# Optimization experiments

Hardware: AMD Instinct MI355X
Metric: run time of the kernel (lower is better)

The kernel has to match this reference:

```python
import jax, jax.numpy as jnp
import numpy as np

D = 768        # d_model
NH = 12        # n_head
HD = D // NH   # head_dim = 64
T = 8          # num_frames
SCALE = 1.0
LN_EPS = 1e-5


def _layer_norm(x, g, b):
    # fp16-safe LayerNorm: compute in fp32, cast back (matches LayerNorm subclass)
    x32 = x.astype(jnp.float32)
    mu = jnp.mean(x32, axis=-1, keepdims=True)
    var = jnp.mean(jnp.square(x32 - mu), axis=-1, keepdims=True)
    y = (x32 - mu) / jnp.sqrt(var + LN_EPS) * g + b
    return y.astype(x.dtype)


def _adapter(x, w1, b1, w2, b2):
    # Adapter with skip_connect=False: fc1 -> exact GELU -> fc2
    h = jax.nn.gelu(x @ w1.T + b1, approximate=False)
    return h @ w2.T + b2


def _mha(xq, ykv, w_in, b_in, w_out, b_out, need_weights=False):
    # xq: (Tx, N, D), ykv: (Ty, N, D); manual in-proj split like the torch code
    q = xq @ w_in[:D].T + b_in[:D]
    k = ykv @ w_in[D:2 * D].T + b_in[D:2 * D]
    v = ykv @ w_in[2 * D:].T + b_in[2 * D:]
    Tx, N = q.shape[0], q.shape[1]
    Ty = k.shape[0]
    q = q.reshape(Tx, N, NH, HD).transpose(1, 2, 0, 3)  # (N, H, Tx, hd)
    k = k.reshape(Ty, N, NH, HD).transpose(1, 2, 0, 3)
    v = v.reshape(Ty, N, NH, HD).transpose(1, 2, 0, 3)
    aff = jnp.einsum('nhqd,nhkd->nhqk', q, k) / jnp.asarray(HD ** 0.5, q.dtype)
    if need_weights:
        # torch does this under no_grad: sum over heads, exp, sum over (Tx*Ty)
        w = jax.lax.stop_gradient(
            jnp.sum(jnp.exp(jnp.sum(aff, axis=1)).reshape(N, -1), axis=-1))
    p = jax.nn.softmax(aff, axis=-1)
    out = jnp.einsum('nhqk,nhkd->nhqd', p, v)
    out = out.transpose(2, 0, 1, 3).reshape(Tx, N, D)
    out = out @ w_out.T + b_out
    if need_weights:
        return out, w
    return out


def setup_inputs() -> dict:
    key = jax.random.key(0)
    ks = jax.random.split(key, 12)
    DH = D // 4  # adapter hidden = 192

    def w(k, shape):
        return jax.random.normal(k, shape, jnp.float32) * 0.02

    z = lambda *s: jnp.zeros(s, jnp.float32)
    return {
        'x': jax.random.normal(ks[0], (197, 64, D), jnp.float32),
        'in_proj_w': w(ks[1], (3 * D, D)), 'in_proj_b': z(3 * D),
        'out_proj_w': w(ks[2], (D, D)), 'out_proj_b': z(D),
        'ln1_g': jnp.ones((D,), jnp.float32), 'ln1_b': z(D),
        'ln2_g': jnp.ones((D,), jnp.float32), 'ln2_b': z(D),
        'fc_w': w(ks[3], (4 * D, D)), 'fc_b': z(4 * D),
        'proj_w': w(ks[4], (D, 4 * D)), 'proj_b': z(D),
        'sa1_w': w(ks[5], (DH, D)), 'sa1_b': z(DH),
        'sa2_w': w(ks[6], (D, DH)), 'sa2_b': z(D),
        'ta1_w': w(ks[7], (DH, D)), 'ta1_b': z(DH),
        'ta2_w': w(ks[8], (D, DH)), 'ta2_b': z(D),
        'ma1_w': w(ks[9], (DH, D)), 'ma1_b': z(DH),
        'ma2_w': w(ks[10], (D, DH)), 'ma2_b': z(D),
    }


def reference(x, in_proj_w, in_proj_b, out_proj_w, out_proj_b,
              ln1_g, ln1_b, ln2_g, ln2_b, fc_w, fc_b, proj_w, proj_b,
              sa1_w, sa1_b, sa2_w, sa2_b, ta1_w, ta1_b, ta2_w, ta2_b,
              ma1_w, ma1_b, ma2_w, ma2_b):
    n, bt, d = x.shape
    b = bt // T
    # temporal attention on the class token: 'n (b t) d -> t (b n) d'
    ct = x[0]                                   # (bt, d)
    xt = ct.reshape(b, T, d).transpose(1, 0, 2)  # (T, b, d)
    xt = _mha(_layer_norm(xt, ln1_g, ln1_b), _layer_norm(xt, ln1_g, ln1_b),
              in_proj_w, in_proj_b, out_proj_w, out_proj_b)
    xt = _adapter(xt, ta1_w, ta1_b, ta2_w, ta2_b)
    xt = xt.transpose(1, 0, 2).reshape(1, bt, d)  # 't (b n) d -> n (b t) d'

    xln = _layer_norm(x, ln1_g, ln1_b)
    ori_attn, ori_w = _mha(xln, xln, in_proj_w, in_proj_b,
                           out_proj_w, out_proj_b, need_weights=True)
    crs_attn, crs_w = _mha(xln, xt, in_proj_w, in_proj_b,
                           out_proj_w, out_proj_b, need_weights=True)
    lam = (crs_w / (crs_w + ori_w))[None, :, None]  # (1, bt, 1)
    x = x + (1.0 - lam) * ori_attn \
          + SCALE * _adapter(lam * crs_attn, sa1_w, sa1_b, sa2_w, sa2_b)

    xn = _layer_norm(x, ln2_g, ln2_b)
    h = xn @ fc_w.T + fc_b
    h = h * jax.nn.sigmoid(1.702 * h)  # QuickGELU
    mlp_out = h @ proj_w.T + proj_b
    x = x + mlp_out + SCALE * _adapter(xn, ma1_w, ma1_b, ma2_w, ma2_b)
    return x
```

## Files before the change

kernel.cpp:

```cpp
#include <hip/hip_runtime.h>
#include <hip/hip_bf16.h>
#include <math.h>


typedef __attribute__((ext_vector_type(8))) short bf16x8;
typedef __attribute__((ext_vector_type(4))) float f32x4;

__device__ __forceinline__ float bf2f(short s) {
  unsigned u = ((unsigned)(unsigned short)s) << 16;
  float f;
  __builtin_memcpy(&f, &u, 4);
  return f;
}
__device__ __forceinline__ short f2bf(float f) {
  __hip_bfloat16 h = __float2bfloat16(f);
  short s;
  __builtin_memcpy(&s, &h, 2);
  return s;
}

__device__ __forceinline__ void gld16(void* lds, const void* g) {
  __builtin_amdgcn_global_load_lds(
      (const __attribute__((address_space(1))) unsigned int*)g,
      (__attribute__((address_space(3))) unsigned int*)lds, 16, 0, 0);
}

struct WPair { const float* s; short* d; int n; };
struct WArr { WPair p[10]; };

__global__ __launch_bounds__(256)
void convert_k(WArr a) {
  WPair w = a.p[blockIdx.y];
  for (int i = blockIdx.x * 256 + threadIdx.x; i < w.n; i += gridDim.x * 256)
    w.d[i] = f2bf(w.s[i]);
}

__global__ __launch_bounds__(256)
void ln_k(const float* __restrict__ in, const float* __restrict__ g,
          const float* __restrict__ b, short* __restrict__ out) {
  const int t = blockIdx.x;
  const float* xr = in + (size_t)t * 768;
  const int tid = threadIdx.x;
  float v0 = xr[tid], v1 = xr[tid + 256], v2 = xr[tid + 512];
  float s = v0 + v1 + v2;
#pragma unroll
  for (int m = 1; m < 64; m <<= 1) s += __shfl_xor(s, m);
  __shared__ float red[4];
  if ((tid & 63) == 0) red[tid >> 6] = s;
  __syncthreads();
  float mu = (red[0] + red[1] + red[2] + red[3]) * (1.f / 768.f);
  __syncthreads();
  float d0 = v0 - mu, d1 = v1 - mu, d2 = v2 - mu;
  float q = d0 * d0 + d1 * d1 + d2 * d2;
#pragma unroll
  for (int m = 1; m < 64; m <<= 1) q += __shfl_xor(q, m);
  if ((tid & 63) == 0) red[tid >> 6] = q;
  __syncthreads();
  float rstd = rsqrtf((red[0] + red[1] + red[2] + red[3]) * (1.f / 768.f) + 1e-5f);
  size_t o = (size_t)t * 768;
  out[o + tid]       = f2bf(d0 * rstd * g[tid]       + b[tid]);
  out[o + tid + 256] = f2bf(d1 * rstd * g[tid + 256] + b[tid + 256]);
  out[o + tid + 512] = f2bf(d2 * rstd * g[tid + 512] + b[tid + 512]);
}

template <int ACT, int EPI>
__global__ __launch_bounds__(256)
void gemm_k(const short* __restrict__ A, int lda,
            const short* __restrict__ W,
            const float* __restrict__ bias,
            short* __restrict__ outb, float* __restrict__ outf,
            const float* __restrict__ lam,
            int M, int N, int K) {
  __shared__ short As[64][40];
  __shared__ short Ws[64][40];
  const int tid = threadIdx.x;
  const int n0 = blockIdx.x * 64;
  const int m0 = blockIdx.y * 64;
  const int lane = tid & 63, w = tid >> 6;
  const int wr = w >> 1, wc = w & 1;
  const int g = lane >> 4, li = lane & 15;
  const int srow = tid >> 2, scol = (tid & 3) * 8;

  f32x4 acc[2][2];
#pragma unroll
  for (int i = 0; i < 2; i++)
#pragma unroll
    for (int j = 0; j < 2; j++) acc[i][j] = (f32x4){0.f, 0.f, 0.f, 0.f};

  const short* Aptr = A + (size_t)(m0 + srow) * lda + scol;
  const short* Wptr = W + (size_t)(n0 + srow) * K + scol;

  for (int kk = 0; kk < K; kk += 32) {
    __syncthreads();
    *(bf16x8*)&As[srow][scol] = *(const bf16x8*)(Aptr + kk);
    *(bf16x8*)&Ws[srow][scol] = *(const bf16x8*)(Wptr + kk);
    __syncthreads();
    bf16x8 a[2], b[2];
#pragma unroll
    for (int mi = 0; mi < 2; ++mi)
      a[mi] = *(const bf16x8*)&As[wr * 32 + mi * 16 + li][g * 8];
#pragma unroll
    for (int ni = 0; ni < 2; ++ni)
      b[ni] = *(const bf16x8*)&Ws[wc * 32 + ni * 16 + li][g * 8];
#pragma unroll
    for (int mi = 0; mi < 2; ++mi)
#pragma unroll
      for (int ni = 0; ni < 2; ++ni)
        acc[mi][ni] = __builtin_amdgcn_mfma_f32_16x16x32_bf16(
            a[mi], b[ni], acc[mi][ni], 0, 0, 0);
  }

#pragma unroll
  for (int mi = 0; mi < 2; ++mi)
#pragma unroll
    for (int ni = 0; ni < 2; ++ni)
#pragma unroll
      for (int r = 0; r < 4; ++r) {
        int row = m0 + wr * 32 + mi * 16 + g * 4 + r;
        int col = n0 + wc * 32 + ni * 16 + li;
        float v = acc[mi][ni][r];
        if (bias) v += bias[col];
        if (ACT == 1) v = v / (1.f + __expf(-1.702f * v));
        if (ACT == 2) v = 0.5f * v * (1.f + erff(v * 0.70710678118f));
        size_t idx = (size_t)row * N + col;
        if (EPI == 0) outb[idx] = f2bf(v);
        else if (EPI == 1) outf[idx] = v;
        else if (EPI == 5) outb[idx] = f2bf(v * lam[row]);
      }
}

template <int ACT, int EPI>
__global__ __launch_bounds__(256)
void gemm128p_k(const short* __restrict__ A, int lda,
                const short* __restrict__ W,
                const float* __restrict__ bias,
                short* __restrict__ outb, float* __restrict__ outf,
                const float* __restrict__ lam,
                const float* __restrict__ addv,
                const float* __restrict__ resid,
                const short* __restrict__ A2, int lda2,
                const short* __restrict__ W2,
                const float* __restrict__ bias2, int K2,
                int M, int N, int K, int nx) {
  int nwg = gridDim.x;
  int orig = blockIdx.x;
  int q = nwg >> 3, r = nwg & 7;
  int xcd = orig & 7, cidx = orig >> 3;
  int wgid = (xcd < r ? xcd * (q + 1) : r * (q + 1) + (xcd - r) * q) + cidx;
  const int n0 = (wgid % nx) * 128;
  const int m0 = (wgid / nx) * 128;

  __shared__ short As[3][128][32];
  __shared__ short Ws[3][128][32];
  const int tid = threadIdx.x;
  const int w = tid >> 6, lane = tid & 63;
  const int g = lane >> 4, li = lane & 15;
  const int wr = w >> 1, wc = w & 1;

  const int srow = w * 16 + (lane >> 2);
  const int scol = (lane & 3) * 8;

  f32x4 acc[4][4];
#pragma unroll
  for (int i = 0; i < 4; i++)
#pragma unroll
    for (int j = 0; j < 4; j++) acc[i][j] = (f32x4){0.f, 0.f, 0.f, 0.f};

  int ar0 = m0 + srow;       if (ar0 > M - 1) ar0 = M - 1;
  int ar1 = m0 + 64 + srow;  if (ar1 > M - 1) ar1 = M - 1;
  const short* Ap0 = A + (size_t)ar0 * lda + scol;
  const short* Ap1 = A + (size_t)ar1 * lda + scol;
  const short* Wp0 = W + (size_t)(n0 + srow) * K + scol;
  const short* Wp1 = W + (size_t)(n0 + 64 + srow) * K + scol;
  const short* A2b = A2 ? A2 : A;
  const short* W2b = W2 ? W2 : W;
  const short* Bp0 = A2b + (size_t)ar0 * lda2 + scol;
  const short* Bp1 = A2b + (size_t)ar1 * lda2 + scol;
  const short* Vp0 = W2b + (size_t)(n0 + srow) * K2 + scol;
  const short* Vp1 = W2b + (size_t)(n0 + 64 + srow) * K2 + scol;

  const int ks1 = K >> 5;
  const int ks2 = A2 ? (K2 >> 5) : 0;
  const int total = ks1 + ks2;

  auto STAGE = [&](int s, int bi) {
    if (s < ks1) {
      const int kk = s * 32;
      gld16(&As[bi][w * 16][0],      Ap0 + kk);
      gld16(&As[bi][64 + w * 16][0], Ap1 + kk);
      gld16(&Ws[bi][w * 16][0],      Wp0 + kk);
      gld16(&Ws[bi][64 + w * 16][0], Wp1 + kk);
    } else {
      const int kk = (s - ks1) * 32;
      gld16(&As[bi][w * 16][0],      Bp0 + kk);
      gld16(&As[bi][64 + w * 16][0], Bp1 + kk);
      gld16(&Ws[bi][w * 16][0],      Vp0 + kk);
      gld16(&Ws[bi][64 + w * 16][0], Vp1 + kk);
    }
  };

  STAGE(0, 0);
  STAGE(1, 1);

  int bi = 0;
  for (int t = 0; t < total; ++t) {
    if (t + 1 < total)
      asm volatile("s_waitcnt vmcnt(4)" ::: "memory");
    else
      asm volatile("s_waitcnt vmcnt(0)" ::: "memory");
    __builtin_amdgcn_s_barrier();

    int nb = bi + 2; if (nb >= 3) nb -= 3;
    if (t + 2 < total) STAGE(t + 2, nb);

    bf16x8 a[4], b[4];
#pragma unroll
    for (int mi = 0; mi < 4; ++mi)
      a[mi] = *(const bf16x8*)&As[bi][wr * 64 + mi * 16 + li][g * 8];
#pragma unroll
    for (int ni = 0; ni < 4; ++ni)
      b[ni] = *(const bf16x8*)&Ws[bi][wc * 64 + ni * 16 + li][g * 8];
    asm volatile("s_waitcnt lgkmcnt(0)" ::: "memory");
    __builtin_amdgcn_sched_barrier(0);
#pragma unroll
    for (int mi = 0; mi < 4; ++mi)
#pragma unroll
      for (int ni = 0; ni < 4; ++ni)
        acc[mi][ni] = __builtin_amdgcn_mfma_f32_16x16x32_bf16(
            a[mi], b[ni], acc[mi][ni], 0, 0, 0);

    bi = bi + 1; if (bi >= 3) bi = 0;
  }

#pragma unroll
  for (int mi = 0; mi < 4; ++mi)
#pragma unroll
    for (int ni = 0; ni < 4; ++ni)
#pragma unroll
      for (int r = 0; r < 4; ++r) {
        int row = m0 + wr * 64 + mi * 16 + g * 4 + r;
        int col = n0 + wc * 64 + ni * 16 + li;
        if (row >= M) continue;
        float v = acc[mi][ni][r];
        if (bias) v += bias[col];
        if (bias2) v += bias2[col];
        if (ACT == 1) v = v / (1.f + __expf(-1.702f * v));
        if (ACT == 2) v = 0.5f * v * (1.f + erff(v * 0.70710678118f));
        size_t idx = (size_t)row * N + col;
        if (EPI == 0) outb[idx] = f2bf(v);
        else if (EPI == 2) {
          float l = lam[row & 63];
          outf[idx] = resid[idx] + (1.f - l) * v + addv[(size_t)(row & 63) * 768 + col];
        } else if (EPI == 6) outf[idx] = resid[idx] + v;
      }
}

__global__ __launch_bounds__(256)
void attn_k(const short* __restrict__ qkv, short* __restrict__ attn_out) {
  const int n = blockIdx.x;
  const int h = blockIdx.y;
  const int tid = threadIdx.x;
  const int lane = tid & 63, w = tid >> 6;
  const int g = lane >> 4, li = lane & 15;

  __shared__ short Vt[64][232];
  __shared__ short Pl[4][16][232];

  {
    const int d = tid & 63;
    for (int key = tid >> 6; key < 224; key += 4) {
      short v = 0;
      if (key < 197)
        v = qkv[(size_t)(key * 64 + n) * 2304 + 1536 + h * 64 + d];
      Vt[d][key] = v;
    }
  }
  __syncthreads();

  const short* Qb = qkv + (size_t)n * 2304 + h * 64;
  const short* Kb = Qb + 768;

  for (int mt = w; mt < 13; mt += 4) {
    const int m0 = mt * 16;
    int arow = m0 + li;
    if (arow > 196) arow = 196;
    bf16x8 a0 = *(const bf16x8*)(Qb + (size_t)arow * 147456 + g * 8);
    bf16x8 a1 = *(const bf16x8*)(Qb + (size_t)arow * 147456 + 32 + g * 8);

    float s[13][4];
#pragma unroll
    for (int nt = 0; nt < 13; ++nt) {
      int kc = nt * 16 + li;
      if (kc > 196) kc = 196;
      bf16x8 b0 = *(const bf16x8*)(Kb + (size_t)kc * 147456 + g * 8);
      bf16x8 b1 = *(const bf16x8*)(Kb + (size_t)kc * 147456 + 32 + g * 8);
      f32x4 acc = (f32x4){0.f, 0.f, 0.f, 0.f};
      acc = __builtin_amdgcn_mfma_f32_16x16x32_bf16(a0, b0, acc, 0, 0, 0);
      acc = __builtin_amdgcn_mfma_f32_16x16x32_bf16(a1, b1, acc, 0, 0, 0);
#pragma unroll
      for (int r = 0; r < 4; ++r) s[nt][r] = acc[r] * 0.125f;
    }

#pragma unroll
    for (int r = 0; r < 4; ++r) {
      float mx = -1e30f;
#pragma unroll
      for (int nt = 0; nt < 13; ++nt) {
        if (nt * 16 + li >= 197) s[nt][r] = -1e30f;
        mx = fmaxf(mx, s[nt][r]);
      }
      mx = fmaxf(mx, __shfl_xor(mx, 1));
      mx = fmaxf(mx, __shfl_xor(mx, 2));
      mx = fmaxf(mx, __shfl_xor(mx, 4));
      mx = fmaxf(mx, __shfl_xor(mx, 8));
      float sum = 0.f;
#pragma unroll
      for (int nt = 0; nt < 13; ++nt) {
        float e = (s[nt][r] <= -1e29f) ? 0.f : __expf(s[nt][r] - mx);
        s[nt][r] = e;
        sum += e;
      }
      sum += __shfl_xor(sum, 1);
      sum += __shfl_xor(sum, 2);
      sum += __shfl_xor(sum, 4);
      sum += __shfl_xor(sum, 8);
      float inv = 1.f / sum;
#pragma unroll
      for (int nt = 0; nt < 13; ++nt) s[nt][r] *= inv;
    }

#pragma unroll
    for (int r = 0; r < 4; ++r) {
      int row = g * 4 + r;
#pragma unroll
      for (int nt = 0; nt < 13; ++nt)
        Pl[w][row][nt * 16 + li] = f2bf(s[nt][r]);
      Pl[w][row][208 + li] = 0;
    }
    asm volatile("s_waitcnt lgkmcnt(0)" ::: "memory");
    __builtin_amdgcn_sched_barrier(0);

    f32x4 o[4];
#pragma unroll
    for (int ni = 0; ni < 4; ++ni) o[ni] = (f32x4){0.f, 0.f, 0.f, 0.f};
#pragma unroll
    for (int kk = 0; kk < 7; ++kk) {
      bf16x8 pa = *(const bf16x8*)&Pl[w][li][kk * 32 + g * 8];
#pragma unroll
      for (int ni = 0; ni < 4; ++ni) {
        bf16x8 vb = *(const bf16x8*)&Vt[ni * 16 + li][kk * 32 + g * 8];
        o[ni] = __builtin_amdgcn_mfma_f32_16x16x32_bf16(pa, vb, o[ni], 0, 0, 0);
      }
    }
#pragma unroll
    for (int ni = 0; ni < 4; ++ni)
#pragma unroll
      for (int r = 0; r < 4; ++r) {
        int prow = m0 + g * 4 + r;
        if (prow < 197)
          attn_out[(size_t)(prow * 64 + n) * 768 + h * 64 + ni * 16 + li] =
              f2bf(o[ni][r]);
      }
  }
}

__global__ __launch_bounds__(256)
void lam_part_k(const short* __restrict__ qkv, float* __restrict__ eo_part) {
  const int n = blockIdx.x;
  const int mt = blockIdx.y;
  const int tid = threadIdx.x;
  const int lane = tid & 63, w = tid >> 6;
  const int g = lane >> 4, li = lane & 15;
  const short* Qb = qkv + (size_t)n * 2304;
  const short* Kb = Qb + 768;

  int arow = mt * 16 + li;
  if (arow > 196) arow = 196;
  const short* Ap = Qb + (size_t)arow * 147456;

  bf16x8 a[24];
#pragma unroll
  for (int s = 0; s < 24; ++s)
    a[s] = *(const bf16x8*)(Ap + s * 32 + g * 8);

  float eo = 0.f;
  for (int nt = w; nt < 13; nt += 4) {
    int kc = nt * 16 + li;
    if (kc > 196) kc = 196;
    const short* Bp = Kb + (size_t)kc * 147456;
    f32x4 acc = (f32x4){0.f, 0.f, 0.f, 0.f};
#pragma unroll
    for (int s = 0; s < 24; ++s) {
      bf16x8 b = *(const bf16x8*)(Bp + s * 32 + g * 8);
      acc = __builtin_amdgcn_mfma_f32_16x16x32_bf16(a[s], b, acc, 0, 0, 0);
    }
#pragma unroll
    for (int r = 0; r < 4; ++r) {
      int prow = mt * 16 + g * 4 + r;
      int col = nt * 16 + li;
      if (prow < 197 && col < 197) eo += __expf(acc[r] * 0.125f);
    }
  }

#pragma unroll
  for (int m = 1; m < 64; m <<= 1) eo += __shfl_xor(eo, m);
  __shared__ float red[4];
  if (lane == 0) red[w] = eo;
  __syncthreads();
  if (tid == 0)
    eo_part[n * 13 + mt] = red[0] + red[1] + red[2] + red[3];
}

__global__ __launch_bounds__(64)
void lam_fin_k(const short* __restrict__ qkv, const short* __restrict__ kvt,
               const float* __restrict__ eo_part, float* __restrict__ lam) {
  const int n = blockIdx.x;
  const int lane = threadIdx.x;
  const short* kt = kvt + (size_t)n * 1536;

  float ec = 0.f;
  for (int p = lane; p < 197; p += 64) {
    const short* qp = qkv + (size_t)n * 2304 + (size_t)p * 147456;
    float dot = 0.f;
    for (int d0 = 0; d0 < 768; d0 += 8) {
      bf16x8 qa = *(const bf16x8*)(qp + d0);
      bf16x8 ka = *(const bf16x8*)(kt + d0);
#pragma unroll
      for (int j = 0; j < 8; ++j) dot += bf2f(qa[j]) * bf2f(ka[j]);
    }
    ec += __expf(dot * 0.125f);
  }
#pragma unroll
  for (int m = 1; m < 64; m <<= 1) ec += __shfl_xor(ec, m);

  if (lane == 0) {
    float eo = 0.f;
#pragma unroll
    for (int t = 0; t < 13; ++t) eo += eo_part[n * 13 + t];
    lam[n] = ec / (ec + eo);
  }
}

__global__ __launch_bounds__(64)
void tattn_k(const short* __restrict__ qkv, short* __restrict__ attn_t) {
  const int bb = blockIdx.x, h = blockIdx.y;
  const int tid = threadIdx.x;
  __shared__ float sm[8][9];
  {
    const int tt = tid >> 3, ss = tid & 7;
    const short* q = qkv + (size_t)(bb * 8 + tt) * 2304 + h * 64;
    const short* k = qkv + (size_t)(bb * 8 + ss) * 2304 + 768 + h * 64;
    float dot = 0.f;
#pragma unroll
    for (int d = 0; d < 64; d += 8) {
      bf16x8 qa = *(const bf16x8*)(q + d);
      bf16x8 ka = *(const bf16x8*)(k + d);
#pragma unroll
      for (int j = 0; j < 8; ++j) dot += bf2f(qa[j]) * bf2f(ka[j]);
    }
    sm[tt][ss] = dot * 0.125f;
  }
  __syncthreads();
  if (tid < 8) {
    float mx = -1e30f;
#pragma unroll
    for (int s2 = 0; s2 < 8; ++s2) mx = fmaxf(mx, sm[tid][s2]);
    float sum = 0.f;
#pragma unroll
    for (int s2 = 0; s2 < 8; ++s2) {
      float e = __expf(sm[tid][s2] - mx);
      sm[tid][s2] = e;
      sum += e;
    }
    float inv = 1.f / sum;
#pragma unroll
    for (int s2 = 0; s2 < 8; ++s2) sm[tid][s2] *= inv;
  }
  __syncthreads();
  {
    const int d = tid;
    float v[8];
#pragma unroll
    for (int s2 = 0; s2 < 8; ++s2)
      v[s2] = bf2f(qkv[(size_t)(bb * 8 + s2) * 2304 + 1536 + h * 64 + d]);
#pragma unroll
    for (int tt = 0; tt < 8; ++tt) {
      float o = 0.f;
#pragma unroll
      for (int s2 = 0; s2 < 8; ++s2) o += sm[tt][s2] * v[s2];
      attn_t[(size_t)(bb * 8 + tt) * 768 + h * 64 + d] = f2bf(o);
    }
  }
}

extern "C" void kernel_launch(void* const* d_in, const int* in_sizes, int n_in,
                              void* d_out, int out_size, void* d_ws,
                              size_t ws_size, hipStream_t stream) {
  (void)in_sizes; (void)n_in; (void)out_size; (void)ws_size;

  const float* x          = (const float*)d_in[0];
  const float* in_proj_w  = (const float*)d_in[1];
  const float* in_proj_b  = (const float*)d_in[2];
  const float* out_proj_w = (const float*)d_in[3];
  const float* out_proj_b = (const float*)d_in[4];
  const float* ln1_g      = (const float*)d_in[5];
  const float* ln1_b      = (const float*)d_in[6];
  const float* ln2_g      = (const float*)d_in[7];
  const float* ln2_b      = (const float*)d_in[8];
  const float* fc_w       = (const float*)d_in[9];
  const float* fc_b       = (const float*)d_in[10];
  const float* proj_w     = (const float*)d_in[11];
  const float* proj_b     = (const float*)d_in[12];
  const float* sa1_w      = (const float*)d_in[13];
  const float* sa1_b      = (const float*)d_in[14];
  const float* sa2_w      = (const float*)d_in[15];
  const float* sa2_b      = (const float*)d_in[16];
  const float* ta1_w      = (const float*)d_in[17];
  const float* ta1_b      = (const float*)d_in[18];
  const float* ta2_w      = (const float*)d_in[19];
  const float* ta2_b      = (const float*)d_in[20];
  const float* ma1_w      = (const float*)d_in[21];
  const float* ma1_b      = (const float*)d_in[22];
  const float* ma2_w      = (const float*)d_in[23];
  const float* ma2_b      = (const float*)d_in[24];

  char* ws = (char*)d_ws;
  short* xln  = (short*)(ws + 0);
  short* qkv  = (short*)(ws + 19365888);
  short* hbuf = (short*)(ws + 0);
  short* attn = (short*)(ws + 77463552);
  short* h2   = (short*)(ws + 77463552);
  float* x1   = (float*)(ws + 96829440);
  short* xn   = (short*)(ws + 135561216);

  char* wreg = ws + 154927104;
  short* w_inproj  = (short*)(wreg + 0);
  short* w_outproj = (short*)(wreg + 3538944);
  short* w_fc      = (short*)(wreg + 4718592);
  short* w_proj    = (short*)(wreg + 9437184);
  short* w_sa1     = (short*)(wreg + 14155776);
  short* w_sa2     = (short*)(wreg + 14450688);
  short* w_ta1     = (short*)(wreg + 14745600);
  short* w_ta2     = (short*)(wreg + 15040512);
  short* w_ma1     = (short*)(wreg + 15335424);
  short* w_ma2     = (short*)(wreg + 15630336);

  char* sm = ws + 170852352;
  short* attn_t  = (short*)(sm + 0);
  short* tproj   = (short*)(sm + 98304);
  short* th      = (short*)(sm + 196608);
  short* xt_out  = (short*)(sm + 221184);
  short* kv_t    = (short*)(sm + 319488);
  short* a_in    = (short*)(sm + 516096);
  short* sa_h    = (short*)(sm + 614400);
  float* sa_out  = (float*)(sm + 638976);
  float* lam     = (float*)(sm + 835584);
  float* eo_part = (float*)(sm + 835840);

  float* out = (float*)d_out;

  WArr arr;
  arr.p[0] = {in_proj_w,  w_inproj,  2304 * 768};
  arr.p[1] = {out_proj_w, w_outproj, 768 * 768};
  arr.p[2] = {fc_w,       w_fc,      3072 * 768};
  arr.p[3] = {proj_w,     w_proj,    768 * 3072};
  arr.p[4] = {sa1_w,      w_sa1,     192 * 768};
  arr.p[5] = {sa2_w,      w_sa2,     768 * 192};
  arr.p[6] = {ta1_w,      w_ta1,     192 * 768};
  arr.p[7] = {ta2_w,      w_ta2,     768 * 192};
  arr.p[8] = {ma1_w,      w_ma1,     192 * 768};
  arr.p[9] = {ma2_w,      w_ma2,     768 * 192};
  convert_k<<<dim3(128, 10), 256, 0, stream>>>(arr);

  ln_k<<<12608, 256, 0, stream>>>(x, ln1_g, ln1_b, xln);

  gemm128p_k<0, 0><<<18 * 99, 256, 0, stream>>>(
      xln, 768, w_inproj, in_proj_b, qkv, nullptr, nullptr, nullptr, nullptr,
      nullptr, 0, nullptr, nullptr, 32, 12608, 2304, 768, 18);

  lam_part_k<<<dim3(64, 13), 256, 0, stream>>>(qkv, eo_part);

  tattn_k<<<dim3(8, 12), 64, 0, stream>>>(qkv, attn_t);

  gemm_k<0, 0><<<dim3(12, 1), 256, 0, stream>>>(
      attn_t, 768, w_outproj, out_proj_b, tproj, nullptr, nullptr, 64, 768, 768);
  gemm_k<2, 0><<<dim3(3, 1), 256, 0, stream>>>(
      tproj, 768, w_ta1, ta1_b, th, nullptr, nullptr, 64, 192, 768);
  gemm_k<0, 0><<<dim3(12, 1), 256, 0, stream>>>(
      th, 192, w_ta2, ta2_b, xt_out, nullptr, nullptr, 64, 768, 192);
  gemm_k<0, 0><<<dim3(24, 1), 256, 0, stream>>>(
      xt_out, 768, w_inproj + 768 * 768, in_proj_b + 768, kv_t, nullptr,
      nullptr, 64, 1536, 768);

  attn_k<<<dim3(64, 12), 256, 0, stream>>>(qkv, attn);

  lam_fin_k<<<64, 64, 0, stream>>>(qkv, kv_t, eo_part, lam);

  gemm_k<0, 5><<<dim3(12, 1), 256, 0, stream>>>(
      kv_t + 768, 1536, w_outproj, out_proj_b, a_in, nullptr, lam, 64, 768, 768);
  gemm_k<2, 0><<<dim3(3, 1), 256, 0, stream>>>(
      a_in, 768, w_sa1, sa1_b, sa_h, nullptr, nullptr, 64, 192, 768);
  gemm_k<0, 1><<<dim3(12, 1), 256, 0, stream>>>(
      sa_h, 192, w_sa2, sa2_b, nullptr, sa_out, nullptr, 64, 768, 192);

  gemm128p_k<0, 2><<<6 * 99, 256, 0, stream>>>(
      attn, 768, w_outproj, out_proj_b, nullptr, x1, lam, sa_out, x,
      nullptr, 0, nullptr, nullptr, 32, 12608, 768, 768, 6);

  ln_k<<<12608, 256, 0, stream>>>(x1, ln2_g, ln2_b, xn);

  gemm128p_k<1, 0><<<24 * 99, 256, 0, stream>>>(
      xn, 768, w_fc, fc_b, hbuf, nullptr, nullptr, nullptr, nullptr,
      nullptr, 0, nullptr, nullptr, 32, 12608, 3072, 768, 24);
  gemm_k<2, 0><<<dim3(3, 197), 256, 0, stream>>>(
      xn, 768, w_ma1, ma1_b, h2, nullptr, nullptr, 12608, 192, 768);

  gemm128p_k<0, 6><<<6 * 99, 256, 0, stream>>>(
      hbuf, 3072, w_proj, proj_b, nullptr, out, nullptr, nullptr, x1,
      h2, 192, w_ma2, ma2_b, 192, 12608, 768, 3072, 6);
}
```

Baseline: 731.5 us.

## Replace 128x128 GEMM with 256x256-tile 8-wave kernel with swizzled LDS

```diff
diff --git a/kernel.cpp b/kernel.cpp
--- a/kernel.cpp
+++ b/kernel.cpp
@@ -130,115 +130,140 @@
 }
 
 template <int ACT, int EPI>
-__global__ __launch_bounds__(256)
-void gemm128p_k(const short* __restrict__ A, int lda,
-                const short* __restrict__ W,
-                const float* __restrict__ bias,
-                short* __restrict__ outb, float* __restrict__ outf,
-                const float* __restrict__ lam,
-                const float* __restrict__ addv,
-                const float* __restrict__ resid,
-                const short* __restrict__ A2, int lda2,
-                const short* __restrict__ W2,
-                const float* __restrict__ bias2, int K2,
-                int M, int N, int K, int nx) {
-  int nwg = gridDim.x;
-  int orig = blockIdx.x;
-  int q = nwg >> 3, r = nwg & 7;
+__global__ __launch_bounds__(512, 2)
+void gemm256_k(const short* __restrict__ A, int lda,
+               const short* __restrict__ W,
+               const float* __restrict__ bias,
+               short* __restrict__ outb, float* __restrict__ outf,
+               const float* __restrict__ lam,
+               const float* __restrict__ addv,
+               const float* __restrict__ resid,
+               const short* __restrict__ A2, int lda2,
+               const short* __restrict__ W2,
+               const float* __restrict__ bias2, int K2t,
+               int M, int N, int Kt, int nx) {
+  constexpr int BUFB = 256 * 64 * 2;
+  __shared__ short As[2][256][64];
+  __shared__ short Ws[2][256][64];
+
+  int nwg = gridDim.x, orig = blockIdx.x;
+  int qq = nwg >> 3, rr = nwg & 7;
   int xcd = orig & 7, cidx = orig >> 3;
-  int wgid = (xcd < r ? xcd * (q + 1) : r * (q + 1) + (xcd - r) * q) + cidx;
-  const int n0 = (wgid % nx) * 128;
-  const int m0 = (wgid / nx) * 128;
-
-  __shared__ short As[3][128][32];
-  __shared__ short Ws[3][128][32];
+  int wgid = (xcd < rr ? xcd * (qq + 1) : rr * (qq + 1) + (xcd - rr) * qq) + cidx;
+  const int n0 = (wgid % nx) * 256;
+  const int m0 = (wgid / nx) * 256;
+
   const int tid = threadIdx.x;
   const int w = tid >> 6, lane = tid & 63;
   const int g = lane >> 4, li = lane & 15;
-  const int wr = w >> 1, wc = w & 1;
-
-  const int srow = w * 16 + (lane >> 2);
-  const int scol = (lane & 3) * 8;
-
-  f32x4 acc[4][4];
-#pragma unroll
-  for (int i = 0; i < 4; i++)
+  const int wr = w >> 2, wc = w & 3;
+
+  const int srow8 = tid >> 3;
+  const int swzc  = (tid & 7) ^ (srow8 & 7);
+
+  const int cx0 = ((g) ^ (li & 7)) * 16;
+  const int cx1 = ((4 + g) ^ (li & 7)) * 16;
+  const int aRow = (wr * 128 + li) * 128;
+  const int bRow = (wc * 64 + li) * 128;
+  const char* AsB = (const char*)As;
+  const char* WsB = (const char*)Ws;
+
+  f32x4 acc[8][4];
+#pragma unroll
+  for (int i = 0; i < 8; i++)
 #pragma unroll
     for (int j = 0; j < 4; j++) acc[i][j] = (f32x4){0.f, 0.f, 0.f, 0.f};
 
-  int ar0 = m0 + srow;       if (ar0 > M - 1) ar0 = M - 1;
-  int ar1 = m0 + 64 + srow;  if (ar1 > M - 1) ar1 = M - 1;
-  const short* Ap0 = A + (size_t)ar0 * lda + scol;
-  const short* Ap1 = A + (size_t)ar1 * lda + scol;
-  const short* Wp0 = W + (size_t)(n0 + srow) * K + scol;
-  const short* Wp1 = W + (size_t)(n0 + 64 + srow) * K + scol;
-  const short* A2b = A2 ? A2 : A;
-  const short* W2b = W2 ? W2 : W;
-  const short* Bp0 = A2b + (size_t)ar0 * lda2 + scol;
-  const short* Bp1 = A2b + (size_t)ar1 * lda2 + scol;
-  const short* Vp0 = W2b + (size_t)(n0 + srow) * K2 + scol;
-  const short* Vp1 = W2b + (size_t)(n0 + 64 + srow) * K2 + scol;
-
-  const int ks1 = K >> 5;
-  const int ks2 = A2 ? (K2 >> 5) : 0;
-  const int total = ks1 + ks2;
-
-  auto STAGE = [&](int s, int bi) {
-    if (s < ks1) {
-      const int kk = s * 32;
-      gld16(&As[bi][w * 16][0],      Ap0 + kk);
-      gld16(&As[bi][64 + w * 16][0], Ap1 + kk);
-      gld16(&Ws[bi][w * 16][0],      Wp0 + kk);
-      gld16(&Ws[bi][64 + w * 16][0], Wp1 + kk);
-    } else {
-      const int kk = (s - ks1) * 32;
-      gld16(&As[bi][w * 16][0],      Bp0 + kk);
-      gld16(&As[bi][64 + w * 16][0], Bp1 + kk);
-      gld16(&Ws[bi][w * 16][0],      Vp0 + kk);
-      gld16(&Ws[bi][64 + w * 16][0], Vp1 + kk);
-    }
+  int arows[2][2], wrows[2][2];
+#pragma unroll
+  for (int h = 0; h < 2; ++h)
+#pragma unroll
+    for (int c = 0; c < 2; ++c) {
+      int rA = m0 + h * 128 + c * 64 + srow8;
+      arows[h][c] = rA > M - 1 ? M - 1 : rA;
+      wrows[h][c] = n0 + h * 128 + c * 64 + srow8;
+    }
+
+  const int ldW1 = Kt * 64, ldW2 = K2t * 64;
+  const int totT = Kt + K2t;
+
+  auto stA = [&](int bb, int s) {
+    const short* bsrc; int ld, k0;
+    if (s < Kt) { bsrc = A;  ld = lda;  k0 = s * 64; }
+    else        { bsrc = A2; ld = lda2; k0 = (s - Kt) * 64; }
+#pragma unroll
+    for (int h = 0; h < 2; ++h)
+#pragma unroll
+      for (int c = 0; c < 2; ++c)
+        gld16((char*)As + bb * BUFB + h * 16384 + c * 8192 + w * 1024,
+              bsrc + (size_t)arows[h][c] * ld + k0 + swzc * 8);
   };
-
-  STAGE(0, 0);
-  STAGE(1, 1);
-
-  int bi = 0;
-  for (int t = 0; t < total; ++t) {
-    if (t + 1 < total)
-      asm volatile("s_waitcnt vmcnt(4)" ::: "memory");
-    else
-      asm volatile("s_waitcnt vmcnt(0)" ::: "memory");
-    __builtin_amdgcn_s_barrier();
-
-    int nb = bi + 2; if (nb >= 3) nb -= 3;
-    if (t + 2 < total) STAGE(t + 2, nb);
-
-    bf16x8 a[4], b[4];
-#pragma unroll
-    for (int mi = 0; mi < 4; ++mi)
-      a[mi] = *(const bf16x8*)&As[bi][wr * 64 + mi * 16 + li][g * 8];
+  auto stB = [&](int bb, int s) {
+    const short* bsrc; int ld, k0;
+    if (s < Kt) { bsrc = W;  ld = ldW1; k0 = s * 64; }
+    else        { bsrc = W2; ld = ldW2; k0 = (s - Kt) * 64; }
+#pragma unroll
+    for (int h = 0; h < 2; ++h)
+#pragma unroll
+      for (int c = 0; c < 2; ++c)
+        gld16((char*)Ws + bb * BUFB + h * 16384 + c * 8192 + w * 1024,
+              bsrc + (size_t)wrows[h][c] * ld + k0 + swzc * 8);
+  };
+
+  stA(0, 0);
+  stB(0, 0);
+  asm volatile("s_waitcnt vmcnt(0)" ::: "memory");
+  __builtin_amdgcn_s_barrier();
+
+  for (int t = 0; t < totT; ++t) {
+    const int bb = t & 1;
+    const char* Ab = AsB + bb * BUFB;
+    const char* Bb = WsB + bb * BUFB;
+
+    bf16x8 bf[4][2];
+#pragma unroll
+    for (int ni = 0; ni < 4; ++ni) {
+      bf[ni][0] = *(const bf16x8*)(Bb + bRow + ni * 2048 + cx0);
+      bf[ni][1] = *(const bf16x8*)(Bb + bRow + ni * 2048 + cx1);
+    }
+
+#pragma unroll
+    for (int p = 0; p < 4; ++p) {
+      bf16x8 a0k0 = *(const bf16x8*)(Ab + aRow + (2 * p) * 2048 + cx0);
+      bf16x8 a0k1 = *(const bf16x8*)(Ab + aRow + (2 * p) * 2048 + cx1);
+      bf16x8 a1k0 = *(const bf16x8*)(Ab + aRow + (2 * p + 1) * 2048 + cx0);
+      bf16x8 a1k1 = *(const bf16x8*)(Ab + aRow + (2 * p + 1) * 2048 + cx1);
+      if (p == 0 && t + 1 < totT) stA(bb ^ 1, t + 1);
+      if (p == 1 && t + 1 < totT) stB(bb ^ 1, t + 1);
+      __builtin_amdgcn_s_barrier();
+      asm volatile("s_waitcnt lgkmcnt(0)" ::: "memory");
+      __builtin_amdgcn_sched_barrier(0);
+      __builtin_amdgcn_s_setprio(1);
+#pragma unroll
+      for (int ni = 0; ni < 4; ++ni) {
+        acc[2 * p][ni] = __builtin_amdgcn_mfma_f32_16x16x32_bf16(
+            a0k0, bf[ni][0], acc[2 * p][ni], 0, 0, 0);
+        acc[2 * p][ni] = __builtin_amdgcn_mfma_f32_16x16x32_bf16(
+            a0k1, bf[ni][1], acc[2 * p][ni], 0, 0, 0);
+        acc[2 * p + 1][ni] = __builtin_amdgcn_mfma_f32_16x16x32_bf16(
+            a1k0, bf[ni][0], acc[2 * p + 1][ni], 0, 0, 0);
+        acc[2 * p + 1][ni] = __builtin_amdgcn_mfma_f32_16x16x32_bf16(
+            a1k1, bf[ni][1], acc[2 * p + 1][ni], 0, 0, 0);
+      }
+      __builtin_amdgcn_s_setprio(0);
+      if (p == 3 && t + 1 < totT)
+        asm volatile("s_waitcnt vmcnt(0)" ::: "memory");
+      __builtin_amdgcn_s_barrier();
+    }
+  }
+
+#pragma unroll
+  for (int mi = 0; mi < 8; ++mi)
 #pragma unroll
     for (int ni = 0; ni < 4; ++ni)
-      b[ni] = *(const bf16x8*)&Ws[bi][wc * 64 + ni * 16 + li][g * 8];
-    asm volatile("s_waitcnt lgkmcnt(0)" ::: "memory");
-    __builtin_amdgcn_sched_barrier(0);
-#pragma unroll
-    for (int mi = 0; mi < 4; ++mi)
-#pragma unroll
-      for (int ni = 0; ni < 4; ++ni)
-        acc[mi][ni] = __builtin_amdgcn_mfma_f32_16x16x32_bf16(
-            a[mi], b[ni], acc[mi][ni], 0, 0, 0);
-
-    bi = bi + 1; if (bi >= 3) bi = 0;
-  }
-
-#pragma unroll
-  for (int mi = 0; mi < 4; ++mi)
-#pragma unroll
-    for (int ni = 0; ni < 4; ++ni)
 #pragma unroll
       for (int r = 0; r < 4; ++r) {
-        int row = m0 + wr * 64 + mi * 16 + g * 4 + r;
+        int row = m0 + wr * 128 + mi * 16 + g * 4 + r;
         int col = n0 + wc * 64 + ni * 16 + li;
         if (row >= M) continue;
         float v = acc[mi][ni][r];
@@ -574,9 +599,9 @@
 
   ln_k<<<12608, 256, 0, stream>>>(x, ln1_g, ln1_b, xln);
 
-  gemm128p_k<0, 0><<<18 * 99, 256, 0, stream>>>(
+  gemm256_k<0, 0><<<9 * 50, 512, 0, stream>>>(
       xln, 768, w_inproj, in_proj_b, qkv, nullptr, nullptr, nullptr, nullptr,
-      nullptr, 0, nullptr, nullptr, 32, 12608, 2304, 768, 18);
+      nullptr, 0, nullptr, nullptr, 0, 12608, 2304, 12, 9);
 
   lam_part_k<<<dim3(64, 13), 256, 0, stream>>>(qkv, eo_part);
 
@@ -603,19 +628,19 @@
   gemm_k<0, 1><<<dim3(12, 1), 256, 0, stream>>>(
       sa_h, 192, w_sa2, sa2_b, nullptr, sa_out, nullptr, 64, 768, 192);
 
-  gemm128p_k<0, 2><<<6 * 99, 256, 0, stream>>>(
+  gemm256_k<0, 2><<<3 * 50, 512, 0, stream>>>(
       attn, 768, w_outproj, out_proj_b, nullptr, x1, lam, sa_out, x,
-      nullptr, 0, nullptr, nullptr, 32, 12608, 768, 768, 6);
+      nullptr, 0, nullptr, nullptr, 0, 12608, 768, 12, 3);
 
   ln_k<<<12608, 256, 0, stream>>>(x1, ln2_g, ln2_b, xn);
 
-  gemm128p_k<1, 0><<<24 * 99, 256, 0, stream>>>(
+  gemm256_k<1, 0><<<12 * 50, 512, 0, stream>>>(
       xn, 768, w_fc, fc_b, hbuf, nullptr, nullptr, nullptr, nullptr,
-      nullptr, 0, nullptr, nullptr, 32, 12608, 3072, 768, 24);
+      nullptr, 0, nullptr, nullptr, 0, 12608, 3072, 12, 12);
   gemm_k<2, 0><<<dim3(3, 197), 256, 0, stream>>>(
       xn, 768, w_ma1, ma1_b, h2, nullptr, nullptr, 12608, 192, 768);
 
-  gemm128p_k<0, 6><<<6 * 99, 256, 0, stream>>>(
+  gemm256_k<0, 6><<<3 * 50, 512, 0, stream>>>(
       hbuf, 3072, w_proj, proj_b, nullptr, out, nullptr, nullptr, x1,
-      h2, 192, w_ma2, ma2_b, 192, 12608, 768, 3072, 6);
-}
+      h2, 192, w_ma2, ma2_b, 3, 12608, 768, 48, 3);
+}
```

Result: slower. 808.5 us (+10.5%).
